# Kernel optimization log

Measured on AMD Instinct MI355X. Metric: run time of the kernel, lower is better.

## Reference

```python
import jax, jax.numpy as jnp
import numpy as np

LN_EPS = 1e-5   # torch LayerNorm default
EPS = 1e-8      # slot-attention renorm eps
ITERS = 3


def _ln(x, g, b):
    m = jnp.mean(x, axis=-1, keepdims=True)
    v = jnp.mean(jnp.square(x - m), axis=-1, keepdims=True)
    return (x - m) * jax.lax.rsqrt(v + LN_EPS) * g + b


def _gru(x, h, W_ih, W_hh, b_ih, b_hh):
    # torch GRUCell: gates ordered r, z, n; weight_* has shape [3h, in]
    gi = x @ W_ih.T + b_ih
    gh = h @ W_hh.T + b_hh
    ir, iz, inn = jnp.split(gi, 3, axis=-1)
    hr, hz, hn = jnp.split(gh, 3, axis=-1)
    r = jax.nn.sigmoid(ir + hr)
    z = jax.nn.sigmoid(iz + hz)
    n = jnp.tanh(inn + r * hn)
    return (1.0 - z) * n + z * h


def setup_inputs() -> dict:
    key = jax.random.key(0)
    ks = jax.random.split(key, 16)
    b, n, d, n_s = 32, 4096, 256, 8
    h = max(d, 128)  # hidden_dim = max(dim, hidden_dim)
    s = 1.0 / np.sqrt(d)
    inp = {
        "inputs": jax.random.normal(ks[0], (b, n, d), jnp.float32),
        "noise": jax.random.normal(ks[1], (b, n_s, d), jnp.float32),
        "slots_mu": jax.random.normal(ks[2], (1, 1, d), jnp.float32),
        "slots_logsigma": jax.random.normal(ks[3], (1, 1, d), jnp.float32) * 0.1,
        "Wq": jax.random.uniform(ks[4], (d, d), jnp.float32, -s, s),
        "bq": jnp.zeros((d,), jnp.float32),
        "Wk": jax.random.uniform(ks[5], (d, d), jnp.float32, -s, s),
        "bk": jnp.zeros((d,), jnp.float32),
        "Wv": jax.random.uniform(ks[6], (d, d), jnp.float32, -s, s),
        "bv": jnp.zeros((d,), jnp.float32),
        "W_ih": jax.random.uniform(ks[7], (3 * d, d), jnp.float32, -s, s),
        "W_hh": jax.random.uniform(ks[8], (3 * d, d), jnp.float32, -s, s),
        "b_ih": jnp.zeros((3 * d,), jnp.float32),
        "b_hh": jnp.zeros((3 * d,), jnp.float32),
        "W1": jax.random.uniform(ks[9], (h, d), jnp.float32, -s, s),
        "b1": jnp.zeros((h,), jnp.float32),
        "W2": jax.random.uniform(ks[10], (d, h), jnp.float32, -s, s),
        "b2": jnp.zeros((d,), jnp.float32),
        "g_in": jnp.ones((d,), jnp.float32), "be_in": jnp.zeros((d,), jnp.float32),
        "g_sl": jnp.ones((d,), jnp.float32), "be_sl": jnp.zeros((d,), jnp.float32),
        "g_ff": jnp.ones((d,), jnp.float32), "be_ff": jnp.zeros((d,), jnp.float32),
    }
    return inp


def reference(inputs, noise, slots_mu, slots_logsigma, Wq, bq, Wk, bk, Wv, bv,
              W_ih, W_hh, b_ih, b_hh, W1, b1, W2, b2,
              g_in, be_in, g_sl, be_sl, g_ff, be_ff):
    b, n, d = inputs.shape
    scale = d ** (-0.5)
    # reparameterized slot init
    slots = slots_mu + jnp.exp(slots_logsigma) * noise          # [b, n_s, d]
    x = _ln(inputs, g_in, be_in)
    k = x @ Wk.T + bk                                           # [b, n, d]
    v = x @ Wv.T + bv
    attn = None
    for _ in range(ITERS):
        slots_prev = slots
        q = _ln(slots, g_sl, be_sl) @ Wq.T + bq                 # [b, n_s, d]
        dots = jnp.einsum('bid,bjd->bij', q, k) * scale         # [b, n_s, n]
        attn = jax.nn.softmax(dots, axis=1)                     # softmax over SLOTS
        attn_ = attn + EPS
        attn_ = attn_ / jnp.sum(attn_, axis=-1, keepdims=True)  # renorm over inputs
        updates = jnp.einsum('bjd,bij->bid', v, attn_)          # [b, n_s, d]
        slots = _gru(updates.reshape(-1, d), slots_prev.reshape(-1, d),
                     W_ih, W_hh, b_ih, b_hh).reshape(b, -1, d)
        pre = _ln(slots, g_ff, be_ff)
        slots = slots + (jax.nn.relu(pre @ W1.T + b1) @ W2.T + b2)
    return (slots, attn)
```

## Files before the change

kernel.cpp:

```cpp
#include <hip/hip_runtime.h>
#include <hip/hip_fp16.h>
#include <cstdint>
#include <cstddef>


#define NTOK 4096
#define DDIM 256
#define NSLOT 8
#define NBATCH 32
#define NCHK 64
#define SROWS (NBATCH * NSLOT)
#define SCALE 0.0625f
#define LN_EPS_C 1e-5f
#define ATTN_EPS_C 1e-8f

__device__ __forceinline__ void wave_reduce2(float& s, float& ss) {
#pragma unroll
  for (int off = 32; off > 0; off >>= 1) {
    s  += __shfl_down(s, off, 64);
    ss += __shfl_down(ss, off, 64);
  }
}
__device__ __forceinline__ void wave_reduce3(float& a, float& b, float& c) {
#pragma unroll
  for (int off = 32; off > 0; off >>= 1) {
    a += __shfl_down(a, off, 64);
    b += __shfl_down(b, off, 64);
    c += __shfl_down(c, off, 64);
  }
}

__global__ __launch_bounds__(256) void convert_weights_k(
    const float* __restrict__ Wq, const float* __restrict__ Wv,
    const float* __restrict__ Wih, const float* __restrict__ Whh,
    const float* __restrict__ W1, const float* __restrict__ W2,
    const float* __restrict__ Wk, __half* __restrict__ WqT,
    __half* __restrict__ WvT, __half* __restrict__ WihT,
    __half* __restrict__ WhhT, __half* __restrict__ W1T,
    __half* __restrict__ W2T, __half* __restrict__ Wk_h) {
  __shared__ float tile[32][33];
  int bz = blockIdx.x;
  int tx = threadIdx.x & 31, ty = threadIdx.x >> 5;
  if (bz >= 80) {
    int ro = (bz - 80) * 32, cd = blockIdx.y * 32;
#pragma unroll
    for (int p = 0; p < 32; p += 8)
      Wk_h[(size_t)(ro + ty + p) * DDIM + cd + tx] =
          __float2half(Wk[(size_t)(ro + ty + p) * DDIM + cd + tx]);
    return;
  }
  const float* in; __half* out; int O, bo;
  if (bz < 8)       { in = Wq;  out = WqT;  O = 256; bo = bz; }
  else if (bz < 16) { in = Wv;  out = WvT;  O = 256; bo = bz - 8; }
  else if (bz < 40) { in = Wih; out = WihT; O = 768; bo = bz - 16; }
  else if (bz < 64) { in = Whh; out = WhhT; O = 768; bo = bz - 40; }
  else if (bz < 72) { in = W1;  out = W1T;  O = 256; bo = bz - 64; }
  else              { in = W2;  out = W2T;  O = 256; bo = bz - 72; }
  int ro = bo * 32, cd = blockIdx.y * 32;
#pragma unroll
  for (int p = 0; p < 32; p += 8)
    tile[ty + p][tx] = in[(size_t)(ro + ty + p) * DDIM + cd + tx];
  __syncthreads();
#pragma unroll
  for (int p = 0; p < 32; p += 8)
    out[(size_t)(cd + ty + p) * O + ro + tx] = __float2half(tile[tx][ty + p]);
}

__global__ __launch_bounds__(256) void fused_attn_f32_k(
    const float* __restrict__ X, const float* __restrict__ g,
    const float* __restrict__ be, const float* __restrict__ qk,
    const float* __restrict__ C0, const float* __restrict__ Gv,
    float* __restrict__ S_part, __half* __restrict__ u_part,
    __half* __restrict__ xh_out) {
  __shared__ float sx[32][260];
  __shared__ float sqkg[NSLOT][DDIM];
  __shared__ float part[8][10][32];
  __shared__ float sm[32], srd[32];
  __shared__ float sC0[NSLOT], sG[NSLOT], sS[NSLOT];
  int b = blockIdx.x, c = blockIdx.y, t = threadIdx.x;
  int tj = t & 31, qd = t >> 5;
#pragma unroll
  for (int i = 0; i < NSLOT; ++i)
    sqkg[i][t] = qk[((size_t)b * NSLOT + i) * DDIM + t] * g[t];
  if (t < NSLOT) { sC0[t] = C0[b * NSLOT + t]; sG[t] = Gv[b * NSLOT + t]; sS[t] = 0.f; }
  float gt = g[t], bet = be[t];
  float acc[NSLOT] = {};
  const size_t base = (size_t)b * NTOK + (size_t)c * 64;
#pragma unroll
  for (int half = 0; half < 2; ++half) {
    __syncthreads();
#pragma unroll
    for (int it = 0; it < 8; ++it) {
      int e = it * 256 + t;
      int row = e >> 6, c4 = e & 63;
      float4 v = *(const float4*)(X + (base + half * 32 + row) * DDIM + c4 * 4);
      *(float4*)&sx[row][c4 * 4] = v;
    }
    __syncthreads();
    float s = 0.f, ss = 0.f, p[NSLOT] = {};
#pragma unroll
    for (int d4 = 0; d4 < 8; ++d4) {
      float4 xv = *(const float4*)&sx[tj][qd * 32 + d4 * 4];
      s += xv.x + xv.y + xv.z + xv.w;
      ss += xv.x * xv.x + xv.y * xv.y + xv.z * xv.z + xv.w * xv.w;
#pragma unroll
      for (int i = 0; i < NSLOT; ++i) {
        float4 qv = *(const float4*)&sqkg[i][qd * 32 + d4 * 4];
        p[i] += xv.x * qv.x + xv.y * qv.y + xv.z * qv.z + xv.w * qv.w;
      }
    }
#pragma unroll
    for (int i = 0; i < NSLOT; ++i) part[qd][i][tj] = p[i];
    part[qd][8][tj] = s;
    part[qd][9][tj] = ss;
    __syncthreads();
    if (t < 32) {
      float s1 = 0.f, s2 = 0.f;
#pragma unroll
      for (int q2 = 0; q2 < 8; ++q2) { s1 += part[q2][8][t]; s2 += part[q2][9][t]; }
      float m = s1 * (1.f / DDIM);
      float rs = rsqrtf(s2 * (1.f / DDIM) - m * m + LN_EPS_C);
      sm[t] = m;
      srd[t] = rs;
      float dots[NSLOT], mx = -1e30f;
#pragma unroll
      for (int i = 0; i < NSLOT; ++i) {
        float P1 = 0.f;
#pragma unroll
        for (int q2 = 0; q2 < 8; ++q2) P1 += part[q2][i][t];
        dots[i] = rs * (P1 - m * sG[i]) + sC0[i];
        mx = fmaxf(mx, dots[i]);
      }
      float sum = 0.f;
#pragma unroll
      for (int i = 0; i < NSLOT; ++i) { dots[i] = expf(dots[i] - mx); sum += dots[i]; }
      float inv = 1.f / sum;
#pragma unroll
      for (int i = 0; i < NSLOT; ++i) {
        float ae = dots[i] * inv + ATTN_EPS_C;
        part[i][8][t] = ae;
        float ps = ae;
#pragma unroll
        for (int off = 16; off > 0; off >>= 1) ps += __shfl_down(ps, off, 64);
        if (t == 0) sS[i] += ps;
      }
    }
    __syncthreads();
#pragma unroll 8
    for (int jj = 0; jj < 32; ++jj) {
      float x = sx[jj][t];
      float xl = (x - sm[jj]) * srd[jj] * gt + bet;
      xh_out[(base + half * 32 + jj) * DDIM + t] = __float2half(xl);
#pragma unroll
      for (int i = 0; i < NSLOT; ++i) acc[i] = fmaf(xl, part[i][8][jj], acc[i]);
    }
  }
  __half* upb = u_part + (((size_t)b * NCHK + c) * NSLOT) * DDIM + t;
#pragma unroll
  for (int i = 0; i < NSLOT; ++i) upb[(size_t)i * DDIM] = __float2half(acc[i]);
  if (t < NSLOT) S_part[((size_t)b * NCHK + c) * NSLOT + t] = sS[t];
}

__global__ __launch_bounds__(256) void fused_attn_f16_k(
    const __half* __restrict__ xh, const float* __restrict__ qk,
    const float* __restrict__ qkb, float* __restrict__ attn_out,
    float* __restrict__ S_part, __half* __restrict__ u_part, int write_attn) {
  __shared__ __half sx[64][258];
  __shared__ float2 sqkf[NSLOT][128];
  __shared__ float part[4][NSLOT][64];
  __shared__ float sa[NSLOT][64];
  __shared__ float sC0[NSLOT], sS[NSLOT];
  int b = blockIdx.x, c = blockIdx.y, t = threadIdx.x;
  {
    int i = t >> 5, p2 = t & 31;
    const float* qr = qk + ((size_t)b * NSLOT + i) * DDIM;
#pragma unroll
    for (int kk = 0; kk < 4; ++kk) {
      int col = p2 * 4 + kk;
      sqkf[i][col] = make_float2(qr[col * 2], qr[col * 2 + 1]);
    }
  }
  if (t < NSLOT) sC0[t] = qkb[b * NSLOT + t];
  const size_t base = (size_t)b * NTOK + (size_t)c * 64;
#pragma unroll
  for (int it = 0; it < 8; ++it) {
    int e = it * 256 + t;
    int row = e >> 5, c8 = e & 31;
    const __half* src = xh + (base + row) * DDIM + c8 * 8;
    uint4 v = *(const uint4*)src;
    __half2* dst = (__half2*)&sx[row][c8 * 8];
    dst[0] = ((const __half2*)&v)[0];
    dst[1] = ((const __half2*)&v)[1];
    dst[2] = ((const __half2*)&v)[2];
    dst[3] = ((const __half2*)&v)[3];
  }
  __syncthreads();
  int tj = t & 63, qd = t >> 6;
  float p[NSLOT] = {};
  const __half2* xrow = (const __half2*)&sx[tj][qd * 64];
#pragma unroll
  for (int dd2 = 0; dd2 < 32; ++dd2) {
    float2 xf = __half22float2(xrow[dd2]);
#pragma unroll
    for (int i = 0; i < NSLOT; ++i) {
      float2 qf = sqkf[i][qd * 32 + dd2];
      p[i] = fmaf(xf.x, qf.x, fmaf(xf.y, qf.y, p[i]));
    }
  }
#pragma unroll
  for (int i = 0; i < NSLOT; ++i) part[qd][i][tj] = p[i];
  __syncthreads();
  if (t < 64) {
    float dots[NSLOT], mx = -1e30f;
#pragma unroll
    for (int i = 0; i < NSLOT; ++i) {
      dots[i] = part[0][i][t] + part[1][i][t] + part[2][i][t] + part[3][i][t] +
                sC0[i];
      mx = fmaxf(mx, dots[i]);
    }
    float sum = 0.f;
#pragma unroll
    for (int i = 0; i < NSLOT; ++i) { dots[i] = expf(dots[i] - mx); sum += dots[i]; }
    float inv = 1.f / sum;
#pragma unroll
    for (int i = 0; i < NSLOT; ++i) {
      float a = dots[i] * inv;
      if (write_attn)
        attn_out[((size_t)b * NSLOT + i) * NTOK + c * 64 + t] = a;
      float ae = a + ATTN_EPS_C;
      sa[i][t] = ae;
      float ps = ae;
#pragma unroll
      for (int off = 32; off > 0; off >>= 1) ps += __shfl_down(ps, off, 64);
      if (t == 0) sS[i] = ps;
    }
  }
  __syncthreads();
  float acc[NSLOT] = {};
#pragma unroll 8
  for (int jj = 0; jj < 64; ++jj) {
    float x = __half2float(sx[jj][t]);
#pragma unroll
    for (int i = 0; i < NSLOT; ++i) acc[i] = fmaf(x, sa[i][jj], acc[i]);
  }
  __half* upb = u_part + (((size_t)b * NCHK + c) * NSLOT) * DDIM + t;
#pragma unroll
  for (int i = 0; i < NSLOT; ++i) upb[(size_t)i * DDIM] = __float2half(acc[i]);
  if (t < NSLOT) S_part[((size_t)b * NCHK + c) * NSLOT + t] = sS[t];
}

__global__ __launch_bounds__(1024) void slot_update_k(
    const __half* __restrict__ u_part, const float* __restrict__ S_part,
    const float* __restrict__ slots_in, const __half* __restrict__ WvT,
    const float* __restrict__ bv, const __half* __restrict__ WihT,
    const __half* __restrict__ WhhT, const float* __restrict__ b_ih,
    const float* __restrict__ b_hh, const float* __restrict__ g_ff,
    const float* __restrict__ be_ff, const __half* __restrict__ W1T,
    const float* __restrict__ b1, const __half* __restrict__ W2T,
    const float* __restrict__ b2, const float* __restrict__ g_sl,
    const float* __restrict__ be_sl, const __half* __restrict__ WqT,
    const float* __restrict__ bq, const __half* __restrict__ Wk_h,
    const float* __restrict__ bk, const float* __restrict__ g_in,
    const float* __restrict__ be_in, const float* __restrict__ noise,
    const float* __restrict__ mu, const float* __restrict__ logsig,
    float* __restrict__ slots_out, float* __restrict__ qk,
    float* __restrict__ C0, float* __restrict__ qkb_out,
    float* __restrict__ G, int init, int compute_qk) {
  __shared__ float red[4][6][DDIM];
  __shared__ float su[DDIM], sh[DDIM], supd[DDIM], v1[DDIM], v2[DDIM];
  __shared__ float scal[16];
  int r = blockIdx.x, t = threadIdx.x;
  int b = r >> 3, i = r & 7;
  int o = t & 255, ks = t >> 8;
  int lane = t & 63, wid = t >> 6;
  if (init) {
    if (ks == 0) {
      float ns = mu[o] + expf(logsig[o]) * noise[(size_t)r * DDIM + o];
      slots_out[(size_t)r * DDIM + o] = ns;
      v2[o] = ns;
    }
    __syncthreads();
  } else {
    {
      float up = 0.f;
      const __half* upp =
          u_part + (((size_t)b * NCHK + ks * 16) * NSLOT + i) * DDIM + o;
#pragma unroll
      for (int cc = 0; cc < 16; ++cc)
        up += __half2float(upp[(size_t)cc * (NSLOT * DDIM)]);
      red[ks][0][o] = up;
    }
    if (t < 64) {
      float sp = S_part[((size_t)b * NCHK + t) * NSLOT + i];
#pragma unroll
      for (int off = 32; off > 0; off >>= 1) sp += __shfl_down(sp, off, 64);
      if (t == 0) scal[0] = sp;
    }
    if (ks == 0) sh[o] = slots_in[(size_t)r * DDIM + o];
    __syncthreads();
    if (ks == 0) {
      float invS = 1.f / scal[0];
      su[o] = (red[0][0][o] + red[1][0][o] + red[2][0][o] + red[3][0][o]) * invS;
    }
    __syncthreads();
    {
      float p = 0.f;
      const __half* wp = WvT + (size_t)(ks * 64) * DDIM + o;
#pragma unroll 8
      for (int dd = 0; dd < 64; ++dd)
        p = fmaf(su[ks * 64 + dd], __half2float(wp[(size_t)dd * DDIM]), p);
      red[ks][0][o] = p;
    }
    __syncthreads();
    if (ks == 0)
      supd[o] = bv[o] + red[0][0][o] + red[1][0][o] + red[2][0][o] + red[3][0][o];
    __syncthreads();
    {
      float p0 = 0, p1 = 0, p2 = 0, p3 = 0, p4 = 0, p5 = 0;
      const __half* pi = WihT + (size_t)(ks * 64) * (3 * DDIM) + o;
      const __half* ph = WhhT + (size_t)(ks * 64) * (3 * DDIM) + o;
#pragma unroll 4
      for (int dd = 0; dd < 64; ++dd) {
        float ud = supd[ks * 64 + dd], hd = sh[ks * 64 + dd];
        size_t off = (size_t)dd * (3 * DDIM);
        p0 = fmaf(ud, __half2float(pi[off]), p0);
        p1 = fmaf(ud, __half2float(pi[off + DDIM]), p1);
        p2 = fmaf(ud, __half2float(pi[off + 2 * DDIM]), p2);
        p3 = fmaf(hd, __half2float(ph[off]), p3);
        p4 = fmaf(hd, __half2float(ph[off + DDIM]), p4);
        p5 = fmaf(hd, __half2float(ph[off + 2 * DDIM]), p5);
      }
      red[ks][0][o] = p0; red[ks][1][o] = p1; red[ks][2][o] = p2;
      red[ks][3][o] = p3; red[ks][4][o] = p4; red[ks][5][o] = p5;
    }
    __syncthreads();
    if (ks == 0) {
      float air = b_ih[o] + red[0][0][o] + red[1][0][o] + red[2][0][o] + red[3][0][o];
      float aiz = b_ih[DDIM + o] + red[0][1][o] + red[1][1][o] + red[2][1][o] + red[3][1][o];
      float ain = b_ih[2 * DDIM + o] + red[0][2][o] + red[1][2][o] + red[2][2][o] + red[3][2][o];
      float ahr = b_hh[o] + red[0][3][o] + red[1][3][o] + red[2][3][o] + red[3][3][o];
      float ahz = b_hh[DDIM + o] + red[0][4][o] + red[1][4][o] + red[2][4][o] + red[3][4][o];
      float ahn = b_hh[2 * DDIM + o] + red[0][5][o] + red[1][5][o] + red[2][5][o] + red[3][5][o];
      float rg = 1.f / (1.f + expf(-(air + ahr)));
      float zg = 1.f / (1.f + expf(-(aiz + ahz)));
      float ng = tanhf(ain + rg * ahn);
      float nh = (1.f - zg) * ng + zg * sh[o];
      v1[o] = nh;
      float s2 = nh, ss2 = nh * nh;
      wave_reduce2(s2, ss2);
      if (lane == 0) { scal[wid] = s2; scal[4 + wid] = ss2; }
    }
    __syncthreads();
    if (ks == 0) {
      float sS = scal[0] + scal[1] + scal[2] + scal[3];
      float sQ = scal[4] + scal[5] + scal[6] + scal[7];
      float m = sS * (1.f / DDIM);
      float rs = rsqrtf(sQ * (1.f / DDIM) - m * m + LN_EPS_C);
      v2[o] = (v1[o] - m) * rs * g_ff[o] + be_ff[o];
    }
    __syncthreads();
    {
      float p = 0.f;
      const __half* wp = W1T + (size_t)(ks * 64) * DDIM + o;
#pragma unroll 8
      for (int dd = 0; dd < 64; ++dd)
        p = fmaf(v2[ks * 64 + dd], __half2float(wp[(size_t)dd * DDIM]), p);
      red[ks][0][o] = p;
    }
    __syncthreads();
    if (ks == 0)
      su[o] = fmaxf(b1[o] + red[0][0][o] + red[1][0][o] + red[2][0][o] + red[3][0][o], 0.f);
    __syncthreads();
    {
      float p = 0.f;
      const __half* wp = W2T + (size_t)(ks * 64) * DDIM + o;
#pragma unroll 8
      for (int dd = 0; dd < 64; ++dd)
        p = fmaf(su[ks * 64 + dd], __half2float(wp[(size_t)dd * DDIM]), p);
      red[ks][0][o] = p;
    }
    __syncthreads();
    if (ks == 0) {
      float out = v1[o] + b2[o] + red[0][0][o] + red[1][0][o] + red[2][0][o] + red[3][0][o];
      slots_out[(size_t)r * DDIM + o] = out;
      v2[o] = out;
    }
    __syncthreads();
  }
  if (!compute_qk) return;
  if (ks == 0) {
    float x = v2[o];
    float s2 = x, ss2 = x * x;
    wave_reduce2(s2, ss2);
    if (lane == 0) { scal[wid] = s2; scal[4 + wid] = ss2; }
  }
  __syncthreads();
  if (ks == 0) {
    float sS = scal[0] + scal[1] + scal[2] + scal[3];
    float sQ = scal[4] + scal[5] + scal[6] + scal[7];
    float m = sS * (1.f / DDIM);
    float rs = rsqrtf(sQ * (1.f / DDIM) - m * m + LN_EPS_C);
    su[o] = (v2[o] - m) * rs * g_sl[o] + be_sl[o];
  }
  __syncthreads();
  {
    float p = 0.f;
    const __half* wp = WqT + (size_t)(ks * 64) * DDIM + o;
#pragma unroll 8
    for (int dd = 0; dd < 64; ++dd)
      p = fmaf(su[ks * 64 + dd], __half2float(wp[(size_t)dd * DDIM]), p);
    red[ks][0][o] = p;
  }
  __syncthreads();
  if (ks == 0)
    sh[o] = bq[o] + red[0][0][o] + red[1][0][o] + red[2][0][o] + red[3][0][o];
  __syncthreads();
  {
    float p = 0.f;
    const __half* wp = Wk_h + (size_t)(ks * 64) * DDIM + o;
#pragma unroll 8
    for (int dd = 0; dd < 64; ++dd)
      p = fmaf(sh[ks * 64 + dd], __half2float(wp[(size_t)dd * DDIM]), p);
    red[ks][0][o] = p;
  }
  __syncthreads();
  if (ks == 0) {
    float qkv = SCALE * (red[0][0][o] + red[1][0][o] + red[2][0][o] + red[3][0][o]);
    qk[(size_t)r * DDIM + o] = qkv;
    float v0 = sh[o] * bk[o], vG = g_in[o] * qkv, vB = be_in[o] * qkv;
    wave_reduce3(v0, vG, vB);
    if (lane == 0) { scal[wid] = v0; scal[4 + wid] = vG; scal[8 + wid] = vB; }
  }
  __syncthreads();
  if (t == 0) {
    float qkb = SCALE * (scal[0] + scal[1] + scal[2] + scal[3]);
    qkb_out[r] = qkb;
    G[r] = scal[4] + scal[5] + scal[6] + scal[7];
    C0[r] = qkb + scal[8] + scal[9] + scal[10] + scal[11];
  }
}

extern "C" void kernel_launch(void* const* d_in, const int* in_sizes, int n_in,
                              void* d_out, int out_size, void* d_ws,
                              size_t ws_size, hipStream_t stream) {
  const float* inputs   = (const float*)d_in[0];
  const float* noise    = (const float*)d_in[1];
  const float* slots_mu = (const float*)d_in[2];
  const float* slots_ls = (const float*)d_in[3];
  const float* Wq   = (const float*)d_in[4];
  const float* bq   = (const float*)d_in[5];
  const float* Wk   = (const float*)d_in[6];
  const float* bk   = (const float*)d_in[7];
  const float* Wv   = (const float*)d_in[8];
  const float* bv   = (const float*)d_in[9];
  const float* W_ih = (const float*)d_in[10];
  const float* W_hh = (const float*)d_in[11];
  const float* b_ih = (const float*)d_in[12];
  const float* b_hh = (const float*)d_in[13];
  const float* W1   = (const float*)d_in[14];
  const float* b1   = (const float*)d_in[15];
  const float* W2   = (const float*)d_in[16];
  const float* b2   = (const float*)d_in[17];
  const float* g_in = (const float*)d_in[18];
  const float* be_in= (const float*)d_in[19];
  const float* g_sl = (const float*)d_in[20];
  const float* be_sl= (const float*)d_in[21];
  const float* g_ff = (const float*)d_in[22];
  const float* be_ff= (const float*)d_in[23];

  float* out_slots = (float*)d_out;
  float* out_attn  = (float*)d_out + SROWS * DDIM;

  float* w = (float*)d_ws;
  float* slots = w;  w += SROWS * DDIM;
  float* qk = w;     w += SROWS * DDIM;
  float* C0 = w;     w += SROWS;
  float* qkb = w;    w += SROWS;
  float* G = w;      w += SROWS;
  float* S_part = w; w += NBATCH * NCHK * NSLOT;
  __half* h = (__half*)w;
  __half* xh = h;     h += (size_t)NBATCH * NTOK * DDIM;
  __half* u_part = h; h += (size_t)NBATCH * NCHK * NSLOT * DDIM;
  __half* WqT_h = h;  h += DDIM * DDIM;
  __half* WvT_h = h;  h += DDIM * DDIM;
  __half* WihT_h = h; h += DDIM * 3 * DDIM;
  __half* WhhT_h = h; h += DDIM * 3 * DDIM;
  __half* W1T_h = h;  h += DDIM * DDIM;
  __half* W2T_h = h;  h += DDIM * DDIM;
  __half* Wk_h = h;   h += DDIM * DDIM;

  convert_weights_k<<<dim3(88, 8), 256, 0, stream>>>(
      Wq, Wv, W_ih, W_hh, W1, W2, Wk, WqT_h, WvT_h, WihT_h, WhhT_h, W1T_h,
      W2T_h, Wk_h);
  slot_update_k<<<SROWS, 1024, 0, stream>>>(
      u_part, S_part, slots, WvT_h, bv, WihT_h, WhhT_h, b_ih, b_hh, g_ff,
      be_ff, W1T_h, b1, W2T_h, b2, g_sl, be_sl, WqT_h, bq, Wk_h, bk, g_in,
      be_in, noise, slots_mu, slots_ls, slots, qk, C0, qkb, G, 1, 1);
  fused_attn_f32_k<<<dim3(NBATCH, NCHK), 256, 0, stream>>>(
      inputs, g_in, be_in, qk, C0, G, S_part, u_part, xh);
  slot_update_k<<<SROWS, 1024, 0, stream>>>(
      u_part, S_part, slots, WvT_h, bv, WihT_h, WhhT_h, b_ih, b_hh, g_ff,
      be_ff, W1T_h, b1, W2T_h, b2, g_sl, be_sl, WqT_h, bq, Wk_h, bk, g_in,
      be_in, noise, slots_mu, slots_ls, slots, qk, C0, qkb, G, 0, 1);
  fused_attn_f16_k<<<dim3(NBATCH, NCHK), 256, 0, stream>>>(
      xh, qk, qkb, out_attn, S_part, u_part, 0);
  slot_update_k<<<SROWS, 1024, 0, stream>>>(
      u_part, S_part, slots, WvT_h, bv, WihT_h, WhhT_h, b_ih, b_hh, g_ff,
      be_ff, W1T_h, b1, W2T_h, b2, g_sl, be_sl, WqT_h, bq, Wk_h, bk, g_in,
      be_in, noise, slots_mu, slots_ls, slots, qk, C0, qkb, G, 0, 1);
  fused_attn_f16_k<<<dim3(NBATCH, NCHK), 256, 0, stream>>>(
      xh, qk, qkb, out_attn, S_part, u_part, 1);
  slot_update_k<<<SROWS, 1024, 0, stream>>>(
      u_part, S_part, slots, WvT_h, bv, WihT_h, WhhT_h, b_ih, b_hh, g_ff,
      be_ff, W1T_h, b1, W2T_h, b2, g_sl, be_sl, WqT_h, bq, Wk_h, bk, g_in,
      be_in, noise, slots_mu, slots_ls, out_slots, qk, C0, qkb, G, 0, 0);
}
```

Baseline: 236.8 us.

## Split input LayerNorm into standalone prep kernel and halve attention chunk size

Replaces the first-iteration fused fp32 attention kernel with a standalone LayerNorm+fp16 conversion kernel, so all three iterations use the fp16 attention kernel. The attention chunk shrinks from 64 to 32 tokens per block, doubling the grid to give more parallelism, with cross-wave partial reduction via shuffle. The G/C0 precomputation in slot_update is dropped, and the slot update now reduces twice as many partial chunks. The cost is an extra full read of the fp32 inputs plus an extra fp16 pass in iteration one, and more partial-sum traffic.

```diff
diff --git a/kernel.cpp b/kernel.cpp
--- a/kernel.cpp
+++ b/kernel.cpp
@@ -8,8 +8,10 @@
 #define DDIM 256
 #define NSLOT 8
 #define NBATCH 32
-#define NCHK 64
+#define CH 32
+#define NCHK 128
 #define SROWS (NBATCH * NSLOT)
+#define NROWS (NBATCH * NTOK)
 #define SCALE 0.0625f
 #define LN_EPS_C 1e-5f
 #define ATTN_EPS_C 1e-8f
@@ -21,12 +23,11 @@
     ss += __shfl_down(ss, off, 64);
   }
 }
-__device__ __forceinline__ void wave_reduce3(float& a, float& b, float& c) {
+__device__ __forceinline__ void wave_reduce2_xor(float& s, float& ss) {
 #pragma unroll
   for (int off = 32; off > 0; off >>= 1) {
-    a += __shfl_down(a, off, 64);
-    b += __shfl_down(b, off, 64);
-    c += __shfl_down(c, off, 64);
+    s  += __shfl_xor(s, off, 64);
+    ss += __shfl_xor(ss, off, 64);
   }
 }
 
@@ -66,109 +67,35 @@
     out[(size_t)(cd + ty + p) * O + ro + tx] = __float2half(tile[tx][ty + p]);
 }
 
-__global__ __launch_bounds__(256) void fused_attn_f32_k(
+__global__ __launch_bounds__(256) void xh_prep_k(
     const float* __restrict__ X, const float* __restrict__ g,
-    const float* __restrict__ be, const float* __restrict__ qk,
-    const float* __restrict__ C0, const float* __restrict__ Gv,
-    float* __restrict__ S_part, __half* __restrict__ u_part,
-    __half* __restrict__ xh_out) {
-  __shared__ float sx[32][260];
-  __shared__ float sqkg[NSLOT][DDIM];
-  __shared__ float part[8][10][32];
-  __shared__ float sm[32], srd[32];
-  __shared__ float sC0[NSLOT], sG[NSLOT], sS[NSLOT];
-  int b = blockIdx.x, c = blockIdx.y, t = threadIdx.x;
-  int tj = t & 31, qd = t >> 5;
-#pragma unroll
-  for (int i = 0; i < NSLOT; ++i)
-    sqkg[i][t] = qk[((size_t)b * NSLOT + i) * DDIM + t] * g[t];
-  if (t < NSLOT) { sC0[t] = C0[b * NSLOT + t]; sG[t] = Gv[b * NSLOT + t]; sS[t] = 0.f; }
-  float gt = g[t], bet = be[t];
-  float acc[NSLOT] = {};
-  const size_t base = (size_t)b * NTOK + (size_t)c * 64;
-#pragma unroll
-  for (int half = 0; half < 2; ++half) {
-    __syncthreads();
-#pragma unroll
-    for (int it = 0; it < 8; ++it) {
-      int e = it * 256 + t;
-      int row = e >> 6, c4 = e & 63;
-      float4 v = *(const float4*)(X + (base + half * 32 + row) * DDIM + c4 * 4);
-      *(float4*)&sx[row][c4 * 4] = v;
-    }
-    __syncthreads();
-    float s = 0.f, ss = 0.f, p[NSLOT] = {};
-#pragma unroll
-    for (int d4 = 0; d4 < 8; ++d4) {
-      float4 xv = *(const float4*)&sx[tj][qd * 32 + d4 * 4];
-      s += xv.x + xv.y + xv.z + xv.w;
-      ss += xv.x * xv.x + xv.y * xv.y + xv.z * xv.z + xv.w * xv.w;
-#pragma unroll
-      for (int i = 0; i < NSLOT; ++i) {
-        float4 qv = *(const float4*)&sqkg[i][qd * 32 + d4 * 4];
-        p[i] += xv.x * qv.x + xv.y * qv.y + xv.z * qv.z + xv.w * qv.w;
-      }
-    }
-#pragma unroll
-    for (int i = 0; i < NSLOT; ++i) part[qd][i][tj] = p[i];
-    part[qd][8][tj] = s;
-    part[qd][9][tj] = ss;
-    __syncthreads();
-    if (t < 32) {
-      float s1 = 0.f, s2 = 0.f;
-#pragma unroll
-      for (int q2 = 0; q2 < 8; ++q2) { s1 += part[q2][8][t]; s2 += part[q2][9][t]; }
-      float m = s1 * (1.f / DDIM);
-      float rs = rsqrtf(s2 * (1.f / DDIM) - m * m + LN_EPS_C);
-      sm[t] = m;
-      srd[t] = rs;
-      float dots[NSLOT], mx = -1e30f;
-#pragma unroll
-      for (int i = 0; i < NSLOT; ++i) {
-        float P1 = 0.f;
-#pragma unroll
-        for (int q2 = 0; q2 < 8; ++q2) P1 += part[q2][i][t];
-        dots[i] = rs * (P1 - m * sG[i]) + sC0[i];
-        mx = fmaxf(mx, dots[i]);
-      }
-      float sum = 0.f;
-#pragma unroll
-      for (int i = 0; i < NSLOT; ++i) { dots[i] = expf(dots[i] - mx); sum += dots[i]; }
-      float inv = 1.f / sum;
-#pragma unroll
-      for (int i = 0; i < NSLOT; ++i) {
-        float ae = dots[i] * inv + ATTN_EPS_C;
-        part[i][8][t] = ae;
-        float ps = ae;
-#pragma unroll
-        for (int off = 16; off > 0; off >>= 1) ps += __shfl_down(ps, off, 64);
-        if (t == 0) sS[i] += ps;
-      }
-    }
-    __syncthreads();
-#pragma unroll 8
-    for (int jj = 0; jj < 32; ++jj) {
-      float x = sx[jj][t];
-      float xl = (x - sm[jj]) * srd[jj] * gt + bet;
-      xh_out[(base + half * 32 + jj) * DDIM + t] = __float2half(xl);
-#pragma unroll
-      for (int i = 0; i < NSLOT; ++i) acc[i] = fmaf(xl, part[i][8][jj], acc[i]);
-    }
-  }
-  __half* upb = u_part + (((size_t)b * NCHK + c) * NSLOT) * DDIM + t;
-#pragma unroll
-  for (int i = 0; i < NSLOT; ++i) upb[(size_t)i * DDIM] = __float2half(acc[i]);
-  if (t < NSLOT) S_part[((size_t)b * NCHK + c) * NSLOT + t] = sS[t];
+    const float* __restrict__ be, __half* __restrict__ xh) {
+  int row = blockIdx.x * 4 + (threadIdx.x >> 6);
+  int lane = threadIdx.x & 63;
+  float4 a = *(const float4*)(X + (size_t)row * DDIM + lane * 4);
+  float s = a.x + a.y + a.z + a.w;
+  float ss = a.x * a.x + a.y * a.y + a.z * a.z + a.w * a.w;
+  wave_reduce2_xor(s, ss);
+  float m = s * (1.f / DDIM);
+  float rs = rsqrtf(ss * (1.f / DDIM) - m * m + LN_EPS_C);
+  float4 gv = *(const float4*)(g + lane * 4);
+  float4 bev = *(const float4*)(be + lane * 4);
+  union { __half2 h[2]; uint2 u; } pk;
+  pk.h[0] = __floats2half2_rn((a.x - m) * rs * gv.x + bev.x,
+                              (a.y - m) * rs * gv.y + bev.y);
+  pk.h[1] = __floats2half2_rn((a.z - m) * rs * gv.z + bev.z,
+                              (a.w - m) * rs * gv.w + bev.w);
+  *(uint2*)(xh + (size_t)row * DDIM + lane * 4) = pk.u;
 }
 
 __global__ __launch_bounds__(256) void fused_attn_f16_k(
     const __half* __restrict__ xh, const float* __restrict__ qk,
     const float* __restrict__ qkb, float* __restrict__ attn_out,
     float* __restrict__ S_part, __half* __restrict__ u_part, int write_attn) {
-  __shared__ __half sx[64][258];
+  __shared__ __half sx[CH][258];
   __shared__ float2 sqkf[NSLOT][128];
-  __shared__ float part[4][NSLOT][64];
-  __shared__ float sa[NSLOT][64];
+  __shared__ float part[4][NSLOT][CH];
+  __shared__ float sa[NSLOT][CH];
   __shared__ float sC0[NSLOT], sS[NSLOT];
   int b = blockIdx.x, c = blockIdx.y, t = threadIdx.x;
   {
@@ -181,41 +108,45 @@
     }
   }
   if (t < NSLOT) sC0[t] = qkb[b * NSLOT + t];
-  const size_t base = (size_t)b * NTOK + (size_t)c * 64;
-#pragma unroll
-  for (int it = 0; it < 8; ++it) {
+  const size_t base = (size_t)b * NTOK + (size_t)c * CH;
+#pragma unroll
+  for (int it = 0; it < 4; ++it) {
     int e = it * 256 + t;
-    int row = e >> 5, c8 = e & 31;
-    const __half* src = xh + (base + row) * DDIM + c8 * 8;
-    uint4 v = *(const uint4*)src;
-    __half2* dst = (__half2*)&sx[row][c8 * 8];
+    int row = e >> 5, c16 = e & 31;
+    uint4 v = *(const uint4*)(xh + (base + row) * DDIM + c16 * 8);
+    __half2* dst = (__half2*)&sx[row][c16 * 8];
     dst[0] = ((const __half2*)&v)[0];
     dst[1] = ((const __half2*)&v)[1];
     dst[2] = ((const __half2*)&v)[2];
     dst[3] = ((const __half2*)&v)[3];
   }
   __syncthreads();
-  int tj = t & 63, qd = t >> 6;
+  int tj = t & 31, qd = t >> 5;
   float p[NSLOT] = {};
-  const __half2* xrow = (const __half2*)&sx[tj][qd * 64];
-#pragma unroll
-  for (int dd2 = 0; dd2 < 32; ++dd2) {
+  const __half2* xrow = (const __half2*)&sx[tj][qd * 32];
+#pragma unroll
+  for (int dd2 = 0; dd2 < 16; ++dd2) {
     float2 xf = __half22float2(xrow[dd2]);
 #pragma unroll
     for (int i = 0; i < NSLOT; ++i) {
-      float2 qf = sqkf[i][qd * 32 + dd2];
+      float2 qf = sqkf[i][qd * 16 + dd2];
       p[i] = fmaf(xf.x, qf.x, fmaf(xf.y, qf.y, p[i]));
     }
   }
 #pragma unroll
-  for (int i = 0; i < NSLOT; ++i) part[qd][i][tj] = p[i];
-  __syncthreads();
-  if (t < 64) {
+  for (int i = 0; i < NSLOT; ++i) p[i] += __shfl_down(p[i], 32, 64);
+  int w = t >> 6;
+  if ((t & 63) < 32) {
+#pragma unroll
+    for (int i = 0; i < NSLOT; ++i) part[w][i][tj] = p[i];
+  }
+  __syncthreads();
+  if (t < CH) {
     float dots[NSLOT], mx = -1e30f;
 #pragma unroll
     for (int i = 0; i < NSLOT; ++i) {
-      dots[i] = part[0][i][t] + part[1][i][t] + part[2][i][t] + part[3][i][t] +
-                sC0[i];
+      dots[i] = part[0][i][t] + part[1][i][t] + part[2][i][t] +
+                part[3][i][t] + sC0[i];
       mx = fmaxf(mx, dots[i]);
     }
     float sum = 0.f;
@@ -226,19 +157,19 @@
     for (int i = 0; i < NSLOT; ++i) {
       float a = dots[i] * inv;
       if (write_attn)
-        attn_out[((size_t)b * NSLOT + i) * NTOK + c * 64 + t] = a;
+        attn_out[((size_t)b * NSLOT + i) * NTOK + c * CH + t] = a;
       float ae = a + ATTN_EPS_C;
       sa[i][t] = ae;
       float ps = ae;
 #pragma unroll
-      for (int off = 32; off > 0; off >>= 1) ps += __shfl_down(ps, off, 64);
+      for (int off = 16; off > 0; off >>= 1) ps += __shfl_down(ps, off, 32);
       if (t == 0) sS[i] = ps;
     }
   }
   __syncthreads();
   float acc[NSLOT] = {};
-#pragma unroll 8
-  for (int jj = 0; jj < 64; ++jj) {
+#pragma unroll
+  for (int jj = 0; jj < CH; ++jj) {
     float x = __half2float(sx[jj][t]);
 #pragma unroll
     for (int i = 0; i < NSLOT; ++i) acc[i] = fmaf(x, sa[i][jj], acc[i]);
@@ -260,12 +191,10 @@
     const float* __restrict__ b2, const float* __restrict__ g_sl,
     const float* __restrict__ be_sl, const __half* __restrict__ WqT,
     const float* __restrict__ bq, const __half* __restrict__ Wk_h,
-    const float* __restrict__ bk, const float* __restrict__ g_in,
-    const float* __restrict__ be_in, const float* __restrict__ noise,
+    const float* __restrict__ bk, const float* __restrict__ noise,
     const float* __restrict__ mu, const float* __restrict__ logsig,
     float* __restrict__ slots_out, float* __restrict__ qk,
-    float* __restrict__ C0, float* __restrict__ qkb_out,
-    float* __restrict__ G, int init, int compute_qk) {
+    float* __restrict__ qkb_out, int init, int compute_qk) {
   __shared__ float red[4][6][DDIM];
   __shared__ float su[DDIM], sh[DDIM], supd[DDIM], v1[DDIM], v2[DDIM];
   __shared__ float scal[16];
@@ -284,22 +213,22 @@
     {
       float up = 0.f;
       const __half* upp =
-          u_part + (((size_t)b * NCHK + ks * 16) * NSLOT + i) * DDIM + o;
-#pragma unroll
-      for (int cc = 0; cc < 16; ++cc)
+          u_part + (((size_t)b * NCHK + ks * 32) * NSLOT + i) * DDIM + o;
+#pragma unroll
+      for (int cc = 0; cc < 32; ++cc)
         up += __half2float(upp[(size_t)cc * (NSLOT * DDIM)]);
       red[ks][0][o] = up;
     }
-    if (t < 64) {
+    if (t < 128) {
       float sp = S_part[((size_t)b * NCHK + t) * NSLOT + i];
 #pragma unroll
       for (int off = 32; off > 0; off >>= 1) sp += __shfl_down(sp, off, 64);
-      if (t == 0) scal[0] = sp;
+      if ((t & 63) == 0) scal[12 + (t >> 6)] = sp;
     }
     if (ks == 0) sh[o] = slots_in[(size_t)r * DDIM + o];
     __syncthreads();
     if (ks == 0) {
-      float invS = 1.f / scal[0];
+      float invS = 1.f / (scal[12] + scal[13]);
       su[o] = (red[0][0][o] + red[1][0][o] + red[2][0][o] + red[3][0][o]) * invS;
     }
     __syncthreads();
@@ -427,17 +356,13 @@
   if (ks == 0) {
     float qkv = SCALE * (red[0][0][o] + red[1][0][o] + red[2][0][o] + red[3][0][o]);
     qk[(size_t)r * DDIM + o] = qkv;
-    float v0 = sh[o] * bk[o], vG = g_in[o] * qkv, vB = be_in[o] * qkv;
-    wave_reduce3(v0, vG, vB);
-    if (lane == 0) { scal[wid] = v0; scal[4 + wid] = vG; scal[8 + wid] = vB; }
-  }
-  __syncthreads();
-  if (t == 0) {
-    float qkb = SCALE * (scal[0] + scal[1] + scal[2] + scal[3]);
-    qkb_out[r] = qkb;
-    G[r] = scal[4] + scal[5] + scal[6] + scal[7];
-    C0[r] = qkb + scal[8] + scal[9] + scal[10] + scal[11];
-  }
+    float v0 = sh[o] * bk[o], d1 = 0.f;
+    wave_reduce2(v0, d1);
+    if (lane == 0) scal[wid] = v0;
+  }
+  __syncthreads();
+  if (t == 0)
+    qkb_out[r] = SCALE * (scal[0] + scal[1] + scal[2] + scal[3]);
 }
 
 extern "C" void kernel_launch(void* const* d_in, const int* in_sizes, int n_in,
@@ -474,12 +399,10 @@
   float* w = (float*)d_ws;
   float* slots = w;  w += SROWS * DDIM;
   float* qk = w;     w += SROWS * DDIM;
-  float* C0 = w;     w += SROWS;
   float* qkb = w;    w += SROWS;
-  float* G = w;      w += SROWS;
   float* S_part = w; w += NBATCH * NCHK * NSLOT;
   __half* h = (__half*)w;
-  __half* xh = h;     h += (size_t)NBATCH * NTOK * DDIM;
+  __half* xh = h;     h += (size_t)NROWS * DDIM;
   __half* u_part = h; h += (size_t)NBATCH * NCHK * NSLOT * DDIM;
   __half* WqT_h = h;  h += DDIM * DDIM;
   __half* WvT_h = h;  h += DDIM * DDIM;
@@ -494,24 +417,16 @@
       W2T_h, Wk_h);
   slot_update_k<<<SROWS, 1024, 0, stream>>>(
       u_part, S_part, slots, WvT_h, bv, WihT_h, WhhT_h, b_ih, b_hh, g_ff,
-      be_ff, W1T_h, b1, W2T_h, b2, g_sl, be_sl, WqT_h, bq, Wk_h, bk, g_in,
-      be_in, noise, slots_mu, slots_ls, slots, qk, C0, qkb, G, 1, 1);
-  fused_attn_f32_k<<<dim3(NBATCH, NCHK), 256, 0, stream>>>(
-      inputs, g_in, be_in, qk, C0, G, S_part, u_part, xh);
-  slot_update_k<<<SROWS, 1024, 0, stream>>>(
-      u_part, S_part, slots, WvT_h, bv, WihT_h, WhhT_h, b_ih, b_hh, g_ff,
-      be_ff, W1T_h, b1, W2T_h, b2, g_sl, be_sl, WqT_h, bq, Wk_h, bk, g_in,
-      be_in, noise, slots_mu, slots_ls, slots, qk, C0, qkb, G, 0, 1);
-  fused_attn_f16_k<<<dim3(NBATCH, NCHK), 256, 0, stream>>>(
-      xh, qk, qkb, out_attn, S_part, u_part, 0);
-  slot_update_k<<<SROWS, 1024, 0, stream>>>(
-      u_part, S_part, slots, WvT_h, bv, WihT_h, WhhT_h, b_ih, b_hh, g_ff,
-      be_ff, W1T_h, b1, W2T_h, b2, g_sl, be_sl, WqT_h, bq, Wk_h, bk, g_in,
-      be_in, noise, slots_mu, slots_ls, slots, qk, C0, qkb, G, 0, 1);
-  fused_attn_f16_k<<<dim3(NBATCH, NCHK), 256, 0, stream>>>(
-      xh, qk, qkb, out_attn, S_part, u_part, 1);
-  slot_update_k<<<SROWS, 1024, 0, stream>>>(
-      u_part, S_part, slots, WvT_h, bv, WihT_h, WhhT_h, b_ih, b_hh, g_ff,
-      be_ff, W1T_h, b1, W2T_h, b2, g_sl, be_sl, WqT_h, bq, Wk_h, bk, g_in,
-      be_in, noise, slots_mu, slots_ls, out_slots, qk, C0, qkb, G, 0, 0);
-}
+      be_ff, W1T_h, b1, W2T_h, b2, g_sl, be_sl, WqT_h, bq, Wk_h, bk, noise,
+      slots_mu, slots_ls, slots, qk, qkb, 1, 1);
+  xh_prep_k<<<NROWS / 4, 256, 0, stream>>>(inputs, g_in, be_in, xh);
+  for (int it = 0; it < 3; ++it) {
+    fused_attn_f16_k<<<dim3(NBATCH, NCHK), 256, 0, stream>>>(
+        xh, qk, qkb, out_attn, S_part, u_part, (it == 2) ? 1 : 0);
+    float* sout = (it == 2) ? out_slots : slots;
+    slot_update_k<<<SROWS, 1024, 0, stream>>>(
+        u_part, S_part, slots, WvT_h, bv, WihT_h, WhhT_h, b_ih, b_hh, g_ff,
+        be_ff, W1T_h, b1, W2T_h, b2, g_sl, be_sl, WqT_h, bq, Wk_h, bk, noise,
+        slots_mu, slots_ls, sout, qk, qkb, 0, (it == 2) ? 0 : 1);
+  }
+}
```

After: 247.2 us. +4.4%, slower.
